# Performance work log

Hardware: AMD Instinct MI355X
Metric: run time of the kernel (lower is better)

## Reference

```python
import jax, jax.numpy as jnp
import numpy as np

N = 50000      # nodes
E = 800000     # edges
D_IN = 128
D_OUT = 128
R = 8          # relation types
EPS = 1e-12    # F.normalize eps


def setup_inputs() -> dict:
    key = jax.random.key(0)
    ks = jax.random.split(key, 10)
    s_in = 1.0 / np.sqrt(D_IN)
    s_out = 1.0 / np.sqrt(D_OUT)
    return {
        "x": jax.random.normal(ks[0], (N, D_IN), jnp.float32),
        "W1": jax.random.normal(ks[1], (R, D_IN, D_OUT), jnp.float32) * s_in,
        "loopW1": jax.random.normal(ks[2], (D_IN, D_OUT), jnp.float32) * s_in,
        "b1": jax.random.normal(ks[3], (D_OUT,), jnp.float32) * 0.01,
        "W2": jax.random.normal(ks[4], (R, D_OUT, D_OUT), jnp.float32) * s_out,
        "loopW2": jax.random.normal(ks[5], (D_OUT, D_OUT), jnp.float32) * s_out,
        "b2": jax.random.normal(ks[6], (D_OUT,), jnp.float32) * 0.01,
        "src": jax.random.randint(ks[7], (E,), 0, N),
        "dst": jax.random.randint(ks[8], (E,), 0, N),
        "etypes": jax.random.randint(ks[9], (E,), 0, R),
    }


def rel_layer(x, src, dst, etypes, W, loopW, b):
    # transform every node by every relation: [R, N, D_out]
    xw = jnp.einsum('ni,rio->rno', x, W)
    # gather per-edge messages: [E, D_out]
    msg = xw[etypes, src]
    # scatter-add to destination nodes
    agg = jax.ops.segment_sum(msg, dst, num_segments=x.shape[0])
    # self-loop + bias (DGL RelGraphConv defaults)
    return agg + x @ loopW + b


def reference(x, W1, loopW1, b1, W2, loopW2, b2, src, dst, etypes):
    h = jax.nn.relu(rel_layer(x, src, dst, etypes, W1, loopW1, b1))
    h = rel_layer(h, src, dst, etypes, W2, loopW2, b2)
    # F.normalize: row-wise L2, eps=1e-12
    nrm = jnp.maximum(jnp.linalg.norm(h, axis=1, keepdims=True), EPS)
    return h / nrm
```

## Files before the change

### kernel.cpp

```cpp
#include <hip/hip_runtime.h>
#include <hip/hip_bf16.h>

#define D 128
#define CH 4096
#define BM 64

typedef unsigned int u32;
typedef unsigned short u16;
typedef __attribute__((ext_vector_type(8))) short s16x8;
typedef __attribute__((ext_vector_type(4))) float f32x4;
typedef __attribute__((ext_vector_type(2))) float f32x2;

__device__ __forceinline__ float bf2f(u16 u) {
    union { u32 u; float f; } v; v.u = ((u32)u) << 16; return v.f;
}
__device__ __forceinline__ u16 f2bf(float f) {
    union { float f; u32 u; } v; v.f = f;
    return (u16)((v.u + 0x7fffu + ((v.u >> 16) & 1u)) >> 16);
}
__device__ __forceinline__ u32 pack_bf2(float a, float b) {
    __hip_bfloat162 t = __float22bfloat162_rn(make_float2(a, b));
    union { __hip_bfloat162 t; u32 u; } v; v.t = t; return v.u;
}
__device__ __forceinline__ void unpack2(u32 u, float& lo, float& hi) {
    union { u32 u; float f; } a, b;
    a.u = u << 16; b.u = u & 0xffff0000u;
    lo = a.f; hi = b.f;
}

__global__ void detect_dtype(const u16* __restrict__ x, int* __restrict__ flag,
                             int* __restrict__ gcnt, int nbuck) {
    __shared__ int cnt;
    if (threadIdx.x == 0) cnt = 0;
    __syncthreads();
    if ((int)threadIdx.x < nbuck) gcnt[threadIdx.x] = 0;
    u16 u = x[2 * threadIdx.x];
    int e = (u >> 7) & 0xFF;
    if (e >= 96 && e <= 150) atomicAdd(&cnt, 1);
    __syncthreads();
    if (threadIdx.x == 0) *flag = (cnt >= 128) ? 0 : 1;
}

__global__ __launch_bounds__(256)
void to_bf16_all(const void* __restrict__ s0, const void* __restrict__ s1,
                 const void* __restrict__ s2, const void* __restrict__ s3,
                 const void* __restrict__ s4, const void* __restrict__ s5,
                 const void* __restrict__ s6,
                 u16* __restrict__ d0, u16* __restrict__ d1, u16* __restrict__ d2,
                 u16* __restrict__ d3, u16* __restrict__ d4, u16* __restrict__ d5,
                 u16* __restrict__ d6,
                 long long n0, long long n1, long long n2, long long n3,
                 long long n4, long long n5, long long n6,
                 const int* __restrict__ flag)
{
    if (*flag == 0) return;
    long long i = (long long)blockIdx.x * 256 + threadIdx.x;
    const void* s; u16* d; long long off;
    if      (i < n0)                   { s = s0; d = d0; off = i; }
    else if (i < n0+n1)                { s = s1; d = d1; off = i-n0; }
    else if (i < n0+n1+n2)             { s = s2; d = d2; off = i-n0-n1; }
    else if (i < n0+n1+n2+n3)          { s = s3; d = d3; off = i-n0-n1-n2; }
    else if (i < n0+n1+n2+n3+n4)       { s = s4; d = d4; off = i-n0-n1-n2-n3; }
    else if (i < n0+n1+n2+n3+n4+n5)    { s = s5; d = d5; off = i-n0-n1-n2-n3-n4; }
    else if (i < n0+n1+n2+n3+n4+n5+n6) { s = s6; d = d6; off = i-n0-n1-n2-n3-n4-n5; }
    else return;
    d[off] = f2bf(((const float*)s)[off]);
}

__global__ __launch_bounds__(256)
void csr_count(const int* __restrict__ dst, int* __restrict__ gcnt, int E, int nbuck) {
    __shared__ int scnt[256];
    int tid = threadIdx.x;
    scnt[tid] = 0;
    __syncthreads();
    int base = blockIdx.x * CH;
#pragma unroll
    for (int it = 0; it < CH / 256; ++it) {
        int e = base + it * 256 + tid;
        if (e < E) atomicAdd(&scnt[dst[e] >> 8], 1);
    }
    __syncthreads();
    if (tid < nbuck && scnt[tid] > 0) atomicAdd(&gcnt[tid], scnt[tid]);
}

__global__ __launch_bounds__(256)
void csr_scan(const int* __restrict__ gcnt, int* __restrict__ bstart, int* __restrict__ bcur,
              int nbuck, int N_, int E_, int* __restrict__ offs) {
    __shared__ int wpart[4];
    int tid = threadIdx.x, lane = tid & 63, wid = tid >> 6;
    int v = (tid < nbuck) ? gcnt[tid] : 0;
    int s = v;
#pragma unroll
    for (int off = 1; off < 64; off <<= 1) {
        int t = __shfl_up(s, off, 64);
        if (lane >= off) s += t;
    }
    if (lane == 63) wpart[wid] = s;
    __syncthreads();
    int add = 0;
    for (int w = 0; w < wid; ++w) add += wpart[w];
    int excl = add + s - v;
    if (tid <= nbuck) bstart[tid] = excl;
    if (tid < nbuck)  bcur[tid]  = excl;
    if (tid == 0) offs[N_] = E_;
}

__global__ __launch_bounds__(256)
void csr_part(const int* __restrict__ src, const int* __restrict__ dst,
              const int* __restrict__ et, int* __restrict__ bcur,
              u32* __restrict__ ebuf, int E, int N, int nbuck) {
    __shared__ int scnt[256], sbase[256];
    int tid = threadIdx.x;
    scnt[tid] = 0;
    __syncthreads();
    int base = blockIdx.x * CH;
#pragma unroll
    for (int it = 0; it < CH / 256; ++it) {
        int e = base + it * 256 + tid;
        if (e < E) atomicAdd(&scnt[dst[e] >> 8], 1);
    }
    __syncthreads();
    if (tid < nbuck) {
        int c = scnt[tid];
        sbase[tid] = c ? atomicAdd(&bcur[tid], c) : 0;
    }
    __syncthreads();
    scnt[tid] = 0;
    __syncthreads();
#pragma unroll
    for (int it = 0; it < CH / 256; ++it) {
        int e = base + it * 256 + tid;
        if (e >= E) continue;
        int d = dst[e];
        int b = d >> 8;
        int p = sbase[b] + atomicAdd(&scnt[b], 1);
        ebuf[p] = ((u32)(d & 255) << 24) | ((u32)et[e] << 16) | (u32)src[e];
    }
}

__global__ __launch_bounds__(256)
void csr_emit(const u32* __restrict__ ebuf, const int* __restrict__ bstart,
              int* __restrict__ offs, int* __restrict__ rowidx, int N) {
    __shared__ int hist[256], excl[256], cur[256];
    __shared__ int wpart[4];
    int b = blockIdx.x, tid = threadIdx.x;
    int lo = bstart[b], hi = bstart[b + 1];
    hist[tid] = 0; cur[tid] = 0;
    __syncthreads();
    for (int i = lo + tid; i < hi; i += 256) atomicAdd(&hist[ebuf[i] >> 24], 1);
    __syncthreads();
    int lane = tid & 63, wid = tid >> 6;
    int v = hist[tid], s = v;
#pragma unroll
    for (int off = 1; off < 64; off <<= 1) {
        int t = __shfl_up(s, off, 64);
        if (lane >= off) s += t;
    }
    if (lane == 63) wpart[wid] = s;
    __syncthreads();
    int add = 0;
    for (int w = 0; w < wid; ++w) add += wpart[w];
    int e_ = add + s - v;
    excl[tid] = e_;
    int node = (b << 8) + tid;
    if (node < N) offs[node] = lo + e_;
    __syncthreads();
    for (int i = lo + tid; i < hi; i += 256) {
        u32 rec = ebuf[i];
        int dl = rec >> 24;
        int p = lo + excl[dl] + atomicAdd(&cur[dl], 1);
        rowidx[p] = (int)(rec & 0xFFFFFFu);
    }
}

#define ACC8(et_, u_) do { float l_, h_; unpack2((u_), l_, h_);        \
    switch (et_) {                                                     \
    case 0: aL[0] += l_; aH[0] += h_; break;                           \
    case 1: aL[1] += l_; aH[1] += h_; break;                           \
    case 2: aL[2] += l_; aH[2] += h_; break;                           \
    case 3: aL[3] += l_; aH[3] += h_; break;                           \
    case 4: aL[4] += l_; aH[4] += h_; break;                           \
    case 5: aL[5] += l_; aH[5] += h_; break;                           \
    case 6: aL[6] += l_; aH[6] += h_; break;                           \
    default: aL[7] += l_; aH[7] += h_; break; } } while (0)

__global__ __launch_bounds__(256)
void agg_pre(const u16* __restrict__ xc, const u16* __restrict__ xo,
             const int* __restrict__ offs, const int* __restrict__ rowidx,
             u16* __restrict__ s, int N_, int R_, const int* __restrict__ flag)
{
    const u16* x = (*flag != 0) ? xc : xo;
    int node = blockIdx.x * 4 + (threadIdx.x >> 6);
    int lane = threadIdx.x & 63;
    if (node >= N_) return;
    const u32* xr = (const u32*)x;

    float aL[8] = {0.f,0.f,0.f,0.f,0.f,0.f,0.f,0.f};
    float aH[8] = {0.f,0.f,0.f,0.f,0.f,0.f,0.f,0.f};

    int j  = __builtin_amdgcn_readfirstlane(offs[node]);
    int j1 = __builtin_amdgcn_readfirstlane(offs[node + 1]);

    for (; j + 4 <= j1; j += 4) {
        int v0 = __builtin_amdgcn_readfirstlane(rowidx[j + 0]);
        int v1 = __builtin_amdgcn_readfirstlane(rowidx[j + 1]);
        int v2 = __builtin_amdgcn_readfirstlane(rowidx[j + 2]);
        int v3 = __builtin_amdgcn_readfirstlane(rowidx[j + 3]);
        u32 u0 = xr[(size_t)(v0 & 0xffff) * 64 + lane];
        u32 u1 = xr[(size_t)(v1 & 0xffff) * 64 + lane];
        u32 u2 = xr[(size_t)(v2 & 0xffff) * 64 + lane];
        u32 u3 = xr[(size_t)(v3 & 0xffff) * 64 + lane];
        ACC8(v0 >> 16, u0);
        ACC8(v1 >> 16, u1);
        ACC8(v2 >> 16, u2);
        ACC8(v3 >> 16, u3);
    }
    for (; j < j1; ++j) {
        int v = __builtin_amdgcn_readfirstlane(rowidx[j]);
        u32 u = xr[(size_t)(v & 0xffff) * 64 + lane];
        ACC8(v >> 16, u);
    }

    size_t plane = (size_t)N_ * 64;
    u32* sp = (u32*)s + (size_t)node * 64 + lane;
#pragma unroll
    for (int r = 0; r < 8; ++r)
        if (r < R_) sp[(size_t)r * plane] = pack_bf2(aL[r], aH[r]);
}

__global__ __launch_bounds__(256)
void gemm_fused(const u16* __restrict__ s,
                const u16* __restrict__ selfc, const u16* __restrict__ selfo,
                const u16* __restrict__ Wc, const u16* __restrict__ Wo,
                const u16* __restrict__ lWc, const u16* __restrict__ lWo,
                const u16* __restrict__ bc, const u16* __restrict__ bo,
                const int* __restrict__ flag,
                int M, int R_, int mode, void* __restrict__ out)
{
    __shared__ u16 As[BM * 128];
    const bool f = (*flag != 0);
    const u16* self  = f ? selfc : selfo;
    const u16* Wall  = f ? Wc  : Wo;
    const u16* loopW = f ? lWc : lWo;
    const u16* bias  = f ? bc  : bo;

    const int row0 = blockIdx.x * BM;
    const int tid  = threadIdx.x;
    const int lane = tid & 63;
    const int wv   = tid >> 6;
    const int quad = lane >> 4;
    const int l16  = lane & 15;

    f32x4 acc[4][2];
#pragma unroll
    for (int mt = 0; mt < 4; ++mt) { acc[mt][0] = (f32x4)0.f; acc[mt][1] = (f32x4)0.f; }

    const size_t planeE = (size_t)M * D;
    const int r_base = (wv << 2) + (lane >> 4);
    const int ccol   = lane & 15;

    for (int c = 0; c <= R_; ++c) {
        const u16* Ak = (c < R_) ? (s + (size_t)c * planeE) : self;
        const u16* B  = (c < R_) ? (Wall + (size_t)c * D * D) : loopW;

        {
            auto* lds0 = (__attribute__((address_space(3))) char*)As;
            int cg = ccol ^ r_base;
            int rg0 = row0 + r_base;
#pragma unroll
            for (int it = 0; it < 4; ++it) {
                int rg = rg0 + it * 16; if (rg >= M) rg = M - 1;
                const u16* gp = Ak + (size_t)rg * D + cg * 8;
                __builtin_amdgcn_global_load_lds(
                    (const __attribute__((address_space(1))) void*)gp,
                    (__attribute__((address_space(3))) void*)(lds0 + it * 4096 + wv * 1024),
                    16, 0, 0);
            }
        }

        s16x8 bf[4][2];
#pragma unroll
        for (int ks = 0; ks < 4; ++ks)
#pragma unroll
            for (int jj = 0; jj < 8; ++jj) {
                u32 p = *(const u32*)(B + (ks * 32 + quad * 8 + jj) * D + wv * 32 + 2 * l16);
                bf[ks][0][jj] = (short)(p & 0xffffu);
                bf[ks][1][jj] = (short)(p >> 16);
            }

        __syncthreads();

#pragma unroll
        for (int ks = 0; ks < 4; ++ks) {
            const int chunk = (ks * 4 + quad) ^ l16;
#pragma unroll
            for (int mt = 0; mt < 4; ++mt) {
                s16x8 a = *(const s16x8*)(As + (mt * 16 + l16) * D + chunk * 8);
                acc[mt][0] = __builtin_amdgcn_mfma_f32_16x16x32_bf16(a, bf[ks][0], acc[mt][0], 0, 0, 0);
                acc[mt][1] = __builtin_amdgcn_mfma_f32_16x16x32_bf16(a, bf[ks][1], acc[mt][1], 0, 0, 0);
            }
        }
        __syncthreads();
    }

    const int cpair = wv * 16 + l16;
    const float b0 = bf2f(bias[2 * cpair]);
    const float b1 = bf2f(bias[2 * cpair + 1]);

    if (mode == 0) {
        u32* o = (u32*)out;
#pragma unroll
        for (int mt = 0; mt < 4; ++mt)
#pragma unroll
            for (int i = 0; i < 4; ++i) {
                int r = row0 + mt * 16 + quad * 4 + i;
                if (r >= M) continue;
                o[(size_t)r * 64 + cpair] = pack_bf2(fmaxf(acc[mt][0][i] + b0, 0.f),
                                                     fmaxf(acc[mt][1][i] + b1, 0.f));
            }
    } else {
        float pr[4][4];
#pragma unroll
        for (int mt = 0; mt < 4; ++mt)
#pragma unroll
            for (int i = 0; i < 4; ++i) {
                float a0 = acc[mt][0][i] + b0;
                float a1 = acc[mt][1][i] + b1;
                acc[mt][0][i] = a0; acc[mt][1][i] = a1;
                float p = a0 * a0 + a1 * a1;
                p += __shfl_xor(p, 1, 64);
                p += __shfl_xor(p, 2, 64);
                p += __shfl_xor(p, 4, 64);
                p += __shfl_xor(p, 8, 64);
                pr[mt][i] = p;
            }
        float* fs = (float*)As;
        if (l16 == 0) {
#pragma unroll
            for (int mt = 0; mt < 4; ++mt)
#pragma unroll
                for (int i = 0; i < 4; ++i)
                    fs[(mt * 16 + quad * 4 + i) * 4 + wv] = pr[mt][i];
        }
        __syncthreads();
        if (tid < 64) {
            float ssum = fs[tid * 4] + fs[tid * 4 + 1] + fs[tid * 4 + 2] + fs[tid * 4 + 3];
            fs[256 + tid] = 1.f / fmaxf(sqrtf(ssum), 1e-12f);
        }
        __syncthreads();
#pragma unroll
        for (int mt = 0; mt < 4; ++mt)
#pragma unroll
            for (int i = 0; i < 4; ++i) {
                int rl = mt * 16 + quad * 4 + i;
                int r = row0 + rl;
                if (r >= M) continue;
                float sc = fs[256 + rl];
                float a0 = acc[mt][0][i] * sc, a1 = acc[mt][1][i] * sc;
                if (f) {
                    f32x2 w; w[0] = a0; w[1] = a1;
                    ((f32x2*)out)[(size_t)r * 64 + cpair] = w;
                } else {
                    ((u32*)out)[(size_t)r * 64 + cpair] = pack_bf2(a0, a1);
                }
            }
    }
}

static inline size_t align256(size_t x) { return (x + 255) & ~(size_t)255; }

extern "C" void kernel_launch(void* const* d_in, const int* in_sizes, int n_in,
                              void* d_out, int out_size, void* d_ws, size_t ws_size,
                              hipStream_t stream)
{
    const void* x_in   = d_in[0];
    const void* W1_in  = d_in[1];
    const void* lW1_in = d_in[2];
    const void* b1_in  = d_in[3];
    const void* W2_in  = d_in[4];
    const void* lW2_in = d_in[5];
    const void* b2_in  = d_in[6];
    const int* src = (const int*)d_in[7];
    const int* dst = (const int*)d_in[8];
    const int* et  = (const int*)d_in[9];

    const int N = in_sizes[0] / D;
    const int E = in_sizes[7];
    const int R = in_sizes[1] / (D * D);
    const int nbuck = (N + 255) >> 8;

    const long long ND  = (long long)N * D;
    const long long RDD = (long long)R * D * D;
    const long long DDl = (long long)D * D;

    size_t off = 0;
    auto alloc = [&](size_t bytes) { size_t o = off; off = align256(off + bytes); return o; };
    size_t o_flag = alloc(256);
    size_t o_xc   = alloc((size_t)ND * 2);
    size_t o_W1   = alloc((size_t)RDD * 2);
    size_t o_lW1  = alloc((size_t)DDl * 2);
    size_t o_b1   = alloc((size_t)D * 2);
    size_t o_W2   = alloc((size_t)RDD * 2);
    size_t o_lW2  = alloc((size_t)DDl * 2);
    size_t o_b2   = alloc((size_t)D * 2);
    size_t o_h    = alloc((size_t)ND * 2);
    size_t o_offs = alloc((size_t)(N + 1) * 4);
    size_t o_gcnt = alloc(1024);
    size_t o_bst  = alloc(1040 * 4);
    size_t o_bcur = alloc(1024);
    size_t o_ebuf = alloc((size_t)E * 4);
    size_t o_ridx = alloc((size_t)E * 4);
    size_t o_s    = alloc((size_t)R * ND * 2);
    (void)ws_size;

    char* ws = (char*)d_ws;
    int* flag   = (int*)(ws + o_flag);
    u16* x_c    = (u16*)(ws + o_xc);
    u16* W1c    = (u16*)(ws + o_W1);
    u16* lW1c   = (u16*)(ws + o_lW1);
    u16* b1c    = (u16*)(ws + o_b1);
    u16* W2c    = (u16*)(ws + o_W2);
    u16* lW2c   = (u16*)(ws + o_lW2);
    u16* b2c    = (u16*)(ws + o_b2);
    u16* h      = (u16*)(ws + o_h);
    int* offs   = (int*)(ws + o_offs);
    int* gcnt   = (int*)(ws + o_gcnt);
    int* bstart = (int*)(ws + o_bst);
    int* bcur   = (int*)(ws + o_bcur);
    u32* ebuf   = (u32*)(ws + o_ebuf);
    int* rowidx = (int*)(ws + o_ridx);
    u16* sbuf   = (u16*)(ws + o_s);

    dim3 blk(256, 1, 1);
    int mb    = (N + BM - 1) / BM;
    int nblkE = (E + CH - 1) / CH;
    auto cdiv = [](long long n) { return (u32)((n + 255) / 256); };

    detect_dtype<<<dim3(1), blk, 0, stream>>>((const u16*)x_in, flag, gcnt, nbuck);
    long long tot = ND + RDD + DDl + D + RDD + DDl + D;
    to_bf16_all<<<dim3(cdiv(tot)), blk, 0, stream>>>(
        x_in, W1_in, lW1_in, b1_in, W2_in, lW2_in, b2_in,
        x_c, W1c, lW1c, b1c, W2c, lW2c, b2c,
        ND, RDD, DDl, (long long)D, RDD, DDl, (long long)D, flag);

    csr_count<<<dim3(nblkE), blk, 0, stream>>>(dst, gcnt, E, nbuck);
    csr_scan<<<dim3(1), blk, 0, stream>>>(gcnt, bstart, bcur, nbuck, N, E, offs);
    csr_part<<<dim3(nblkE), blk, 0, stream>>>(src, dst, et, bcur, ebuf, E, N, nbuck);
    csr_emit<<<dim3(nbuck), blk, 0, stream>>>(ebuf, bstart, offs, rowidx, N);

    agg_pre<<<dim3((N + 3) / 4), blk, 0, stream>>>(
        x_c, (const u16*)x_in, offs, rowidx, sbuf, N, R, flag);
    gemm_fused<<<dim3(mb), blk, 0, stream>>>(
        sbuf, x_c, (const u16*)x_in, W1c, (const u16*)W1_in, lW1c, (const u16*)lW1_in,
        b1c, (const u16*)b1_in, flag, N, R, 0, h);

    agg_pre<<<dim3((N + 3) / 4), blk, 0, stream>>>(
        h, h, offs, rowidx, sbuf, N, R, flag);
    gemm_fused<<<dim3(mb), blk, 0, stream>>>(
        sbuf, h, h, W2c, (const u16*)W2_in, lW2c, (const u16*)lW2_in,
        b2c, (const u16*)b2_in, flag, N, R, 1, d_out);
}
```

Before: 317.4 us.

## Fuse per-relation aggregation with the GEMM, staging sums in LDS

Merges the aggregation and GEMM kernels into one kernel per layer. Each 128-thread block gathers neighbor features for 32 rows into 8 swizzled LDS relation planes plus the self rows, then runs MFMA over all 9 planes. This removes the global round trip of the R×N×D bf16 intermediate and one launch per layer. In exchange it uses 72KB of LDS per block, which lowers occupancy, and the irregular gather now runs inside the GEMM block with fewer waves to hide latency.

```diff
diff --git a/kernel.cpp b/kernel.cpp
--- a/kernel.cpp
+++ b/kernel.cpp
@@ -3,7 +3,7 @@
 
 #define D 128
 #define CH 4096
-#define BM 64
+#define BM 32
 
 typedef unsigned int u32;
 typedef unsigned short u16;
@@ -184,65 +184,21 @@
     case 6: aL[6] += l_; aH[6] += h_; break;                           \
     default: aL[7] += l_; aH[7] += h_; break; } } while (0)
 
-__global__ __launch_bounds__(256)
-void agg_pre(const u16* __restrict__ xc, const u16* __restrict__ xo,
-             const int* __restrict__ offs, const int* __restrict__ rowidx,
-             u16* __restrict__ s, int N_, int R_, const int* __restrict__ flag)
+__global__ __launch_bounds__(128)
+void rel_layer_fused(const u16* __restrict__ xc, const u16* __restrict__ xo,
+                     const int* __restrict__ offs, const int* __restrict__ rowidx,
+                     const u16* __restrict__ Wc, const u16* __restrict__ Wo,
+                     const u16* __restrict__ lWc, const u16* __restrict__ lWo,
+                     const u16* __restrict__ bc, const u16* __restrict__ bo,
+                     const int* __restrict__ flag,
+                     int M, int R_, int mode, void* __restrict__ out)
 {
-    const u16* x = (*flag != 0) ? xc : xo;
-    int node = blockIdx.x * 4 + (threadIdx.x >> 6);
-    int lane = threadIdx.x & 63;
-    if (node >= N_) return;
-    const u32* xr = (const u32*)x;
-
-    float aL[8] = {0.f,0.f,0.f,0.f,0.f,0.f,0.f,0.f};
-    float aH[8] = {0.f,0.f,0.f,0.f,0.f,0.f,0.f,0.f};
-
-    int j  = __builtin_amdgcn_readfirstlane(offs[node]);
-    int j1 = __builtin_amdgcn_readfirstlane(offs[node + 1]);
-
-    for (; j + 4 <= j1; j += 4) {
-        int v0 = __builtin_amdgcn_readfirstlane(rowidx[j + 0]);
-        int v1 = __builtin_amdgcn_readfirstlane(rowidx[j + 1]);
-        int v2 = __builtin_amdgcn_readfirstlane(rowidx[j + 2]);
-        int v3 = __builtin_amdgcn_readfirstlane(rowidx[j + 3]);
-        u32 u0 = xr[(size_t)(v0 & 0xffff) * 64 + lane];
-        u32 u1 = xr[(size_t)(v1 & 0xffff) * 64 + lane];
-        u32 u2 = xr[(size_t)(v2 & 0xffff) * 64 + lane];
-        u32 u3 = xr[(size_t)(v3 & 0xffff) * 64 + lane];
-        ACC8(v0 >> 16, u0);
-        ACC8(v1 >> 16, u1);
-        ACC8(v2 >> 16, u2);
-        ACC8(v3 >> 16, u3);
-    }
-    for (; j < j1; ++j) {
-        int v = __builtin_amdgcn_readfirstlane(rowidx[j]);
-        u32 u = xr[(size_t)(v & 0xffff) * 64 + lane];
-        ACC8(v >> 16, u);
-    }
-
-    size_t plane = (size_t)N_ * 64;
-    u32* sp = (u32*)s + (size_t)node * 64 + lane;
-#pragma unroll
-    for (int r = 0; r < 8; ++r)
-        if (r < R_) sp[(size_t)r * plane] = pack_bf2(aL[r], aH[r]);
-}
-
-__global__ __launch_bounds__(256)
-void gemm_fused(const u16* __restrict__ s,
-                const u16* __restrict__ selfc, const u16* __restrict__ selfo,
-                const u16* __restrict__ Wc, const u16* __restrict__ Wo,
-                const u16* __restrict__ lWc, const u16* __restrict__ lWo,
-                const u16* __restrict__ bc, const u16* __restrict__ bo,
-                const int* __restrict__ flag,
-                int M, int R_, int mode, void* __restrict__ out)
-{
-    __shared__ u16 As[BM * 128];
+    __shared__ u16 As[9 * BM * D];
     const bool f = (*flag != 0);
-    const u16* self  = f ? selfc : selfo;
-    const u16* Wall  = f ? Wc  : Wo;
+    const u16* X     = f ? xc : xo;
+    const u16* Wall  = f ? Wc : Wo;
     const u16* loopW = f ? lWc : lWo;
-    const u16* bias  = f ? bc  : bo;
+    const u16* bias  = f ? bc : bo;
 
     const int row0 = blockIdx.x * BM;
     const int tid  = threadIdx.x;
@@ -251,117 +207,180 @@
     const int quad = lane >> 4;
     const int l16  = lane & 15;
 
-    f32x4 acc[4][2];
-#pragma unroll
-    for (int mt = 0; mt < 4; ++mt) { acc[mt][0] = (f32x4)0.f; acc[mt][1] = (f32x4)0.f; }
-
-    const size_t planeE = (size_t)M * D;
-    const int r_base = (wv << 2) + (lane >> 4);
-    const int ccol   = lane & 15;
+    {
+        auto* lds0 = (__attribute__((address_space(3))) char*)As;
+#pragma unroll
+        for (int it = 0; it < 4; ++it) {
+            int rl = it * 8 + wv * 4 + quad;
+            int cg = l16 ^ (rl & 15);
+            int rg = row0 + rl; if (rg >= M) rg = M - 1;
+            const u16* gp = X + (size_t)rg * D + cg * 8;
+            __builtin_amdgcn_global_load_lds(
+                (const __attribute__((address_space(1))) void*)gp,
+                (__attribute__((address_space(3))) void*)(lds0 + 65536 + (it * 8 + wv * 4) * 256),
+                16, 0, 0);
+        }
+    }
+
+    {
+        const u32* xr = (const u32*)X;
+        const int gbase = row0 + wv * 16;
+        int idx = gbase + lane; if (idx > M) idx = M;
+        int offv = offs[idx];
+        u32* plane = (u32*)As;
+
+        for (int rr = 0; rr < 16; ++rr) {
+            int j0 = __builtin_amdgcn_readlane(offv, rr);
+            int j1 = __builtin_amdgcn_readlane(offv, rr + 1);
+            float aL[8] = {0.f,0.f,0.f,0.f,0.f,0.f,0.f,0.f};
+            float aH[8] = {0.f,0.f,0.f,0.f,0.f,0.f,0.f,0.f};
+            int nE = j1 - j0;
+            if (nE > 0) {
+                int vcl = j0 + lane; if (vcl > j1 - 1) vcl = j1 - 1;
+                int vrow = rowidx[vcl];
+                int nb = nE < 64 ? nE : 64;
+                int kk = 0;
+                for (; kk + 8 <= nb; kk += 8) {
+                    int i0 = __builtin_amdgcn_readlane(vrow, kk + 0);
+                    int i1 = __builtin_amdgcn_readlane(vrow, kk + 1);
+                    int i2 = __builtin_amdgcn_readlane(vrow, kk + 2);
+                    int i3 = __builtin_amdgcn_readlane(vrow, kk + 3);
+                    int i4 = __builtin_amdgcn_readlane(vrow, kk + 4);
+                    int i5 = __builtin_amdgcn_readlane(vrow, kk + 5);
+                    int i6 = __builtin_amdgcn_readlane(vrow, kk + 6);
+                    int i7 = __builtin_amdgcn_readlane(vrow, kk + 7);
+                    u32 g0 = xr[(size_t)(i0 & 0xffff) * 64 + lane];
+                    u32 g1 = xr[(size_t)(i1 & 0xffff) * 64 + lane];
+                    u32 g2 = xr[(size_t)(i2 & 0xffff) * 64 + lane];
+                    u32 g3 = xr[(size_t)(i3 & 0xffff) * 64 + lane];
+                    u32 g4 = xr[(size_t)(i4 & 0xffff) * 64 + lane];
+                    u32 g5 = xr[(size_t)(i5 & 0xffff) * 64 + lane];
+                    u32 g6 = xr[(size_t)(i6 & 0xffff) * 64 + lane];
+                    u32 g7 = xr[(size_t)(i7 & 0xffff) * 64 + lane];
+                    ACC8(i0 >> 16, g0); ACC8(i1 >> 16, g1);
+                    ACC8(i2 >> 16, g2); ACC8(i3 >> 16, g3);
+                    ACC8(i4 >> 16, g4); ACC8(i5 >> 16, g5);
+                    ACC8(i6 >> 16, g6); ACC8(i7 >> 16, g7);
+                }
+                for (; kk < nb; ++kk) {
+                    int v = __builtin_amdgcn_readlane(vrow, kk);
+                    u32 g = xr[(size_t)(v & 0xffff) * 64 + lane];
+                    ACC8(v >> 16, g);
+                }
+                for (int j = j0 + 64; j < j1; ++j) {
+                    int v = __builtin_amdgcn_readfirstlane(rowidx[j]);
+                    u32 g = xr[(size_t)(v & 0xffff) * 64 + lane];
+                    ACC8(v >> 16, g);
+                }
+            }
+            int rl = wv * 16 + rr;
+            int widx = rl * 64 + (((lane >> 2) ^ rr) << 2) + (lane & 3);
+#pragma unroll
+            for (int r = 0; r < 8; ++r)
+                if (r < R_) plane[r * 2048 + widx] = pack_bf2(aL[r], aH[r]);
+        }
+    }
+
+    __syncthreads();
+
+    f32x4 acc[2][4];
+#pragma unroll
+    for (int mt = 0; mt < 2; ++mt)
+#pragma unroll
+        for (int q = 0; q < 4; ++q) acc[mt][q] = (f32x4)0.f;
 
     for (int c = 0; c <= R_; ++c) {
-        const u16* Ak = (c < R_) ? (s + (size_t)c * planeE) : self;
-        const u16* B  = (c < R_) ? (Wall + (size_t)c * D * D) : loopW;
-
-        {
-            auto* lds0 = (__attribute__((address_space(3))) char*)As;
-            int cg = ccol ^ r_base;
-            int rg0 = row0 + r_base;
-#pragma unroll
-            for (int it = 0; it < 4; ++it) {
-                int rg = rg0 + it * 16; if (rg >= M) rg = M - 1;
-                const u16* gp = Ak + (size_t)rg * D + cg * 8;
-                __builtin_amdgcn_global_load_lds(
-                    (const __attribute__((address_space(1))) void*)gp,
-                    (__attribute__((address_space(3))) void*)(lds0 + it * 4096 + wv * 1024),
-                    16, 0, 0);
+        const u16* B = (c < R_) ? (Wall + (size_t)c * D * D) : loopW;
+        const int pidx = (c < R_) ? c : 8;
+        s16x8 bfr[4][4];
+#pragma unroll
+        for (int ks = 0; ks < 4; ++ks)
+#pragma unroll
+            for (int g = 0; g < 2; ++g)
+#pragma unroll
+                for (int jj = 0; jj < 8; ++jj) {
+                    u32 p = *(const u32*)(B + (ks * 32 + quad * 8 + jj) * D + wv * 64 + g * 32 + 2 * l16);
+                    bfr[ks][2 * g][jj]     = (short)(p & 0xffffu);
+                    bfr[ks][2 * g + 1][jj] = (short)(p >> 16);
+                }
+#pragma unroll
+        for (int ks = 0; ks < 4; ++ks) {
+            const int chp = (ks * 4 + quad) ^ l16;
+#pragma unroll
+            for (int mt = 0; mt < 2; ++mt) {
+                s16x8 a = *(const s16x8*)(As + (pidx * BM + mt * 16 + l16) * D + chp * 8);
+#pragma unroll
+                for (int q = 0; q < 4; ++q)
+                    acc[mt][q] = __builtin_amdgcn_mfma_f32_16x16x32_bf16(a, bfr[ks][q], acc[mt][q], 0, 0, 0);
             }
         }
-
-        s16x8 bf[4][2];
-#pragma unroll
-        for (int ks = 0; ks < 4; ++ks)
-#pragma unroll
-            for (int jj = 0; jj < 8; ++jj) {
-                u32 p = *(const u32*)(B + (ks * 32 + quad * 8 + jj) * D + wv * 32 + 2 * l16);
-                bf[ks][0][jj] = (short)(p & 0xffffu);
-                bf[ks][1][jj] = (short)(p >> 16);
-            }
-
-        __syncthreads();
-
-#pragma unroll
-        for (int ks = 0; ks < 4; ++ks) {
-            const int chunk = (ks * 4 + quad) ^ l16;
-#pragma unroll
-            for (int mt = 0; mt < 4; ++mt) {
-                s16x8 a = *(const s16x8*)(As + (mt * 16 + l16) * D + chunk * 8);
-                acc[mt][0] = __builtin_amdgcn_mfma_f32_16x16x32_bf16(a, bf[ks][0], acc[mt][0], 0, 0, 0);
-                acc[mt][1] = __builtin_amdgcn_mfma_f32_16x16x32_bf16(a, bf[ks][1], acc[mt][1], 0, 0, 0);
-            }
-        }
-        __syncthreads();
-    }
-
-    const int cpair = wv * 16 + l16;
-    const float b0 = bf2f(bias[2 * cpair]);
-    const float b1 = bf2f(bias[2 * cpair + 1]);
+    }
+
+    const int cp0 = wv * 32 + l16;
+    const int cp1 = wv * 32 + 16 + l16;
+    const float b00 = bf2f(bias[2 * cp0]), b01 = bf2f(bias[2 * cp0 + 1]);
+    const float b10 = bf2f(bias[2 * cp1]), b11 = bf2f(bias[2 * cp1 + 1]);
 
     if (mode == 0) {
         u32* o = (u32*)out;
 #pragma unroll
-        for (int mt = 0; mt < 4; ++mt)
+        for (int mt = 0; mt < 2; ++mt)
 #pragma unroll
             for (int i = 0; i < 4; ++i) {
                 int r = row0 + mt * 16 + quad * 4 + i;
                 if (r >= M) continue;
-                o[(size_t)r * 64 + cpair] = pack_bf2(fmaxf(acc[mt][0][i] + b0, 0.f),
-                                                     fmaxf(acc[mt][1][i] + b1, 0.f));
+                o[(size_t)r * 64 + cp0] = pack_bf2(fmaxf(acc[mt][0][i] + b00, 0.f),
+                                                  fmaxf(acc[mt][1][i] + b01, 0.f));
+                o[(size_t)r * 64 + cp1] = pack_bf2(fmaxf(acc[mt][2][i] + b10, 0.f),
+                                                  fmaxf(acc[mt][3][i] + b11, 0.f));
             }
     } else {
-        float pr[4][4];
-#pragma unroll
-        for (int mt = 0; mt < 4; ++mt)
+        float* fs = (float*)As;
+        __syncthreads();
+        float pr[2][4];
+#pragma unroll
+        for (int mt = 0; mt < 2; ++mt)
 #pragma unroll
             for (int i = 0; i < 4; ++i) {
-                float a0 = acc[mt][0][i] + b0;
-                float a1 = acc[mt][1][i] + b1;
+                float a0 = acc[mt][0][i] + b00;
+                float a1 = acc[mt][1][i] + b01;
+                float a2 = acc[mt][2][i] + b10;
+                float a3 = acc[mt][3][i] + b11;
                 acc[mt][0][i] = a0; acc[mt][1][i] = a1;
-                float p = a0 * a0 + a1 * a1;
+                acc[mt][2][i] = a2; acc[mt][3][i] = a3;
+                float p = a0 * a0 + a1 * a1 + a2 * a2 + a3 * a3;
                 p += __shfl_xor(p, 1, 64);
                 p += __shfl_xor(p, 2, 64);
                 p += __shfl_xor(p, 4, 64);
                 p += __shfl_xor(p, 8, 64);
                 pr[mt][i] = p;
             }
-        float* fs = (float*)As;
         if (l16 == 0) {
 #pragma unroll
-            for (int mt = 0; mt < 4; ++mt)
+            for (int mt = 0; mt < 2; ++mt)
 #pragma unroll
                 for (int i = 0; i < 4; ++i)
-                    fs[(mt * 16 + quad * 4 + i) * 4 + wv] = pr[mt][i];
+                    fs[(mt * 16 + quad * 4 + i) * 2 + wv] = pr[mt][i];
         }
         __syncthreads();
-        if (tid < 64) {
-            float ssum = fs[tid * 4] + fs[tid * 4 + 1] + fs[tid * 4 + 2] + fs[tid * 4 + 3];
-            fs[256 + tid] = 1.f / fmaxf(sqrtf(ssum), 1e-12f);
-        }
-        __syncthreads();
-#pragma unroll
-        for (int mt = 0; mt < 4; ++mt)
+#pragma unroll
+        for (int mt = 0; mt < 2; ++mt)
 #pragma unroll
             for (int i = 0; i < 4; ++i) {
                 int rl = mt * 16 + quad * 4 + i;
                 int r = row0 + rl;
                 if (r >= M) continue;
-                float sc = fs[256 + rl];
+                float sc = 1.f / fmaxf(sqrtf(fs[rl * 2] + fs[rl * 2 + 1]), 1e-12f);
                 float a0 = acc[mt][0][i] * sc, a1 = acc[mt][1][i] * sc;
+                float a2 = acc[mt][2][i] * sc, a3 = acc[mt][3][i] * sc;
                 if (f) {
-                    f32x2 w; w[0] = a0; w[1] = a1;
-                    ((f32x2*)out)[(size_t)r * 64 + cpair] = w;
+                    f32x2 w0; w0[0] = a0; w0[1] = a1;
+                    f32x2 w1; w1[0] = a2; w1[1] = a3;
+                    ((f32x2*)out)[(size_t)r * 64 + cp0] = w0;
+                    ((f32x2*)out)[(size_t)r * 64 + cp1] = w1;
                 } else {
-                    ((u32*)out)[(size_t)r * 64 + cpair] = pack_bf2(a0, a1);
+                    ((u32*)out)[(size_t)r * 64 + cp0] = pack_bf2(a0, a1);
+                    ((u32*)out)[(size_t)r * 64 + cp1] = pack_bf2(a2, a3);
                 }
             }
     }
@@ -410,7 +429,6 @@
     size_t o_bcur = alloc(1024);
     size_t o_ebuf = alloc((size_t)E * 4);
     size_t o_ridx = alloc((size_t)E * 4);
-    size_t o_s    = alloc((size_t)R * ND * 2);
     (void)ws_size;
 
     char* ws = (char*)d_ws;
@@ -429,7 +447,6 @@
     int* bcur   = (int*)(ws + o_bcur);
     u32* ebuf   = (u32*)(ws + o_ebuf);
     int* rowidx = (int*)(ws + o_ridx);
-    u16* sbuf   = (u16*)(ws + o_s);
 
     dim3 blk(256, 1, 1);
     int mb    = (N + BM - 1) / BM;
@@ -448,15 +465,13 @@
     csr_part<<<dim3(nblkE), blk, 0, stream>>>(src, dst, et, bcur, ebuf, E, N, nbuck);
     csr_emit<<<dim3(nbuck), blk, 0, stream>>>(ebuf, bstart, offs, rowidx, N);
 
-    agg_pre<<<dim3((N + 3) / 4), blk, 0, stream>>>(
-        x_c, (const u16*)x_in, offs, rowidx, sbuf, N, R, flag);
-    gemm_fused<<<dim3(mb), blk, 0, stream>>>(
-        sbuf, x_c, (const u16*)x_in, W1c, (const u16*)W1_in, lW1c, (const u16*)lW1_in,
+    rel_layer_fused<<<dim3(mb), dim3(128), 0, stream>>>(
+        x_c, (const u16*)x_in, offs, rowidx,
+        W1c, (const u16*)W1_in, lW1c, (const u16*)lW1_in,
         b1c, (const u16*)b1_in, flag, N, R, 0, h);
 
-    agg_pre<<<dim3((N + 3) / 4), blk, 0, stream>>>(
-        h, h, offs, rowidx, sbuf, N, R, flag);
-    gemm_fused<<<dim3(mb), blk, 0, stream>>>(
-        sbuf, h, h, W2c, (const u16*)W2_in, lW2c, (const u16*)lW2_in,
+    rel_layer_fused<<<dim3(mb), dim3(128), 0, stream>>>(
+        h, h, offs, rowidx,
+        W2c, (const u16*)W2_in, lW2c, (const u16*)lW2_in,
         b2c, (const u16*)b2_in, flag, N, R, 1, d_out);
 }
```

Result: slower. 628.2 us (+98.0%).

## Fuse per-relation aggregation into GEMM kernel with etype-sorted CSR and pre-swizzled weights

Applied to the files above, without the earlier changes.

Drops the separate agg_pre kernel and its global per-relation staging buffer. Each rel_layer_fused block now aggregates neighbour features for its 16 rows directly into LDS planes, one per relation, then runs MFMA over the 9 weight matrices. The CSR is additionally sorted by edge type within each destination, so each wave can accumulate runs and flush once per type change. A build_wt kernel pre-swizzles the weights into the MFMA fragment layout so B loads become vectorized. This removes the large bf16 intermediate written and read through HBM, at the cost of smaller GEMM tiles, more LDS per block and serial gather loops per wave.

```diff
diff --git a/kernel.cpp b/kernel.cpp
--- a/kernel.cpp
+++ b/kernel.cpp
@@ -3,7 +3,7 @@
 
 #define D 128
 #define CH 4096
-#define BM 64
+#define BM 16
 
 typedef unsigned int u32;
 typedef unsigned short u16;
@@ -141,16 +141,23 @@
 __global__ __launch_bounds__(256)
 void csr_emit(const u32* __restrict__ ebuf, const int* __restrict__ bstart,
               int* __restrict__ offs, int* __restrict__ rowidx, int N) {
-    __shared__ int hist[256], excl[256], cur[256];
+    __shared__ int hist[2048], excl[2048], cur[2048];
     __shared__ int wpart[4];
     int b = blockIdx.x, tid = threadIdx.x;
     int lo = bstart[b], hi = bstart[b + 1];
-    hist[tid] = 0; cur[tid] = 0;
-    __syncthreads();
-    for (int i = lo + tid; i < hi; i += 256) atomicAdd(&hist[ebuf[i] >> 24], 1);
-    __syncthreads();
+    for (int i = tid; i < 2048; i += 256) { hist[i] = 0; cur[i] = 0; }
+    __syncthreads();
+    for (int i = lo + tid; i < hi; i += 256) {
+        u32 rec = ebuf[i];
+        int key = (int)((rec >> 24) << 3) | (int)((rec >> 16) & 7u);
+        atomicAdd(&hist[key], 1);
+    }
+    __syncthreads();
+    int loc[8]; int tsum = 0;
+#pragma unroll
+    for (int k = 0; k < 8; ++k) { loc[k] = tsum; tsum += hist[tid * 8 + k]; }
     int lane = tid & 63, wid = tid >> 6;
-    int v = hist[tid], s = v;
+    int s = tsum;
 #pragma unroll
     for (int off = 1; off < 64; off <<= 1) {
         int t = __shfl_up(s, off, 64);
@@ -160,89 +167,64 @@
     __syncthreads();
     int add = 0;
     for (int w = 0; w < wid; ++w) add += wpart[w];
-    int e_ = add + s - v;
-    excl[tid] = e_;
+    int tex = add + s - tsum;
+#pragma unroll
+    for (int k = 0; k < 8; ++k) excl[tid * 8 + k] = tex + loc[k];
     int node = (b << 8) + tid;
-    if (node < N) offs[node] = lo + e_;
+    if (node < N) offs[node] = lo + tex;
     __syncthreads();
     for (int i = lo + tid; i < hi; i += 256) {
         u32 rec = ebuf[i];
-        int dl = rec >> 24;
-        int p = lo + excl[dl] + atomicAdd(&cur[dl], 1);
+        int key = (int)((rec >> 24) << 3) | (int)((rec >> 16) & 7u);
+        int p = lo + excl[key] + atomicAdd(&cur[key], 1);
         rowidx[p] = (int)(rec & 0xFFFFFFu);
     }
 }
 
-#define ACC8(et_, u_) do { float l_, h_; unpack2((u_), l_, h_);        \
-    switch (et_) {                                                     \
-    case 0: aL[0] += l_; aH[0] += h_; break;                           \
-    case 1: aL[1] += l_; aH[1] += h_; break;                           \
-    case 2: aL[2] += l_; aH[2] += h_; break;                           \
-    case 3: aL[3] += l_; aH[3] += h_; break;                           \
-    case 4: aL[4] += l_; aH[4] += h_; break;                           \
-    case 5: aL[5] += l_; aH[5] += h_; break;                           \
-    case 6: aL[6] += l_; aH[6] += h_; break;                           \
-    default: aL[7] += l_; aH[7] += h_; break; } } while (0)
-
 __global__ __launch_bounds__(256)
-void agg_pre(const u16* __restrict__ xc, const u16* __restrict__ xo,
-             const int* __restrict__ offs, const int* __restrict__ rowidx,
-             u16* __restrict__ s, int N_, int R_, const int* __restrict__ flag)
+void build_wt(const u16* __restrict__ W1c, const u16* __restrict__ W1o,
+              const u16* __restrict__ lW1c, const u16* __restrict__ lW1o,
+              const u16* __restrict__ W2c, const u16* __restrict__ W2o,
+              const u16* __restrict__ lW2c, const u16* __restrict__ lW2o,
+              const int* __restrict__ flag, int R_, u16* __restrict__ wt)
 {
-    const u16* x = (*flag != 0) ? xc : xo;
-    int node = blockIdx.x * 4 + (threadIdx.x >> 6);
-    int lane = threadIdx.x & 63;
-    if (node >= N_) return;
-    const u32* xr = (const u32*)x;
-
-    float aL[8] = {0.f,0.f,0.f,0.f,0.f,0.f,0.f,0.f};
-    float aH[8] = {0.f,0.f,0.f,0.f,0.f,0.f,0.f,0.f};
-
-    int j  = __builtin_amdgcn_readfirstlane(offs[node]);
-    int j1 = __builtin_amdgcn_readfirstlane(offs[node + 1]);
-
-    for (; j + 4 <= j1; j += 4) {
-        int v0 = __builtin_amdgcn_readfirstlane(rowidx[j + 0]);
-        int v1 = __builtin_amdgcn_readfirstlane(rowidx[j + 1]);
-        int v2 = __builtin_amdgcn_readfirstlane(rowidx[j + 2]);
-        int v3 = __builtin_amdgcn_readfirstlane(rowidx[j + 3]);
-        u32 u0 = xr[(size_t)(v0 & 0xffff) * 64 + lane];
-        u32 u1 = xr[(size_t)(v1 & 0xffff) * 64 + lane];
-        u32 u2 = xr[(size_t)(v2 & 0xffff) * 64 + lane];
-        u32 u3 = xr[(size_t)(v3 & 0xffff) * 64 + lane];
-        ACC8(v0 >> 16, u0);
-        ACC8(v1 >> 16, u1);
-        ACC8(v2 >> 16, u2);
-        ACC8(v3 >> 16, u3);
-    }
-    for (; j < j1; ++j) {
-        int v = __builtin_amdgcn_readfirstlane(rowidx[j]);
-        u32 u = xr[(size_t)(v & 0xffff) * 64 + lane];
-        ACC8(v >> 16, u);
-    }
-
-    size_t plane = (size_t)N_ * 64;
-    u32* sp = (u32*)s + (size_t)node * 64 + lane;
-#pragma unroll
-    for (int r = 0; r < 8; ++r)
-        if (r < R_) sp[(size_t)r * plane] = pack_bf2(aL[r], aH[r]);
-}
-
-__global__ __launch_bounds__(256)
-void gemm_fused(const u16* __restrict__ s,
-                const u16* __restrict__ selfc, const u16* __restrict__ selfo,
-                const u16* __restrict__ Wc, const u16* __restrict__ Wo,
-                const u16* __restrict__ lWc, const u16* __restrict__ lWo,
-                const u16* __restrict__ bc, const u16* __restrict__ bo,
-                const int* __restrict__ flag,
-                int M, int R_, int mode, void* __restrict__ out)
+    __shared__ u32 st[8192];
+    bool f = (*flag != 0);
+    int m = blockIdx.x;
+    int layer = m / 9, c = m % 9;
+    const u16* src;
+    if (layer == 0) src = (c < R_) ? ((f ? W1c : W1o) + (size_t)c * D * D) : (f ? lW1c : lW1o);
+    else            src = (c < R_) ? ((f ? W2c : W2o) + (size_t)c * D * D) : (f ? lW2c : lW2o);
+    int tid = threadIdx.x;
+    const u32* s32 = (const u32*)src;
+    for (int i = tid; i < 8192; i += 256) st[i] = s32[i];
+    __syncthreads();
+    const u16* st16 = (const u16*)st;
+    u16* dstp = wt + (size_t)m * 16384;
+    for (int i = tid; i < 16384; i += 256) {
+        int wvv = i >> 12;
+        int ks  = (i >> 10) & 3;
+        int h   = (i >> 9) & 1;
+        int ln  = (i >> 3) & 63;
+        int j   = i & 7;
+        int k   = ks * 32 + (ln >> 4) * 8 + j;
+        int col = wvv * 32 + 2 * (ln & 15) + h;
+        dstp[i] = st16[k * 128 + col];
+    }
+}
+
+__global__ __launch_bounds__(256, 4)
+void rel_layer_fused(const u16* __restrict__ xc, const u16* __restrict__ xo,
+                     const int* __restrict__ offs, const int* __restrict__ rowidx,
+                     const u16* __restrict__ wt,
+                     const u16* __restrict__ bc, const u16* __restrict__ bo,
+                     const int* __restrict__ flag,
+                     int M, int R_, int mode, void* __restrict__ out)
 {
-    __shared__ u16 As[BM * 128];
+    __shared__ u16 As[9 * BM * D];
     const bool f = (*flag != 0);
-    const u16* self  = f ? selfc : selfo;
-    const u16* Wall  = f ? Wc  : Wo;
-    const u16* loopW = f ? lWc : lWo;
-    const u16* bias  = f ? bc  : bo;
+    const u16* X    = f ? xc : xo;
+    const u16* bias = f ? bc : bo;
 
     const int row0 = blockIdx.x * BM;
     const int tid  = threadIdx.x;
@@ -251,119 +233,183 @@
     const int quad = lane >> 4;
     const int l16  = lane & 15;
 
-    f32x4 acc[4][2];
-#pragma unroll
-    for (int mt = 0; mt < 4; ++mt) { acc[mt][0] = (f32x4)0.f; acc[mt][1] = (f32x4)0.f; }
-
-    const size_t planeE = (size_t)M * D;
-    const int r_base = (wv << 2) + (lane >> 4);
-    const int ccol   = lane & 15;
-
-    for (int c = 0; c <= R_; ++c) {
-        const u16* Ak = (c < R_) ? (s + (size_t)c * planeE) : self;
-        const u16* B  = (c < R_) ? (Wall + (size_t)c * D * D) : loopW;
-
-        {
-            auto* lds0 = (__attribute__((address_space(3))) char*)As;
-            int cg = ccol ^ r_base;
-            int rg0 = row0 + r_base;
-#pragma unroll
-            for (int it = 0; it < 4; ++it) {
-                int rg = rg0 + it * 16; if (rg >= M) rg = M - 1;
-                const u16* gp = Ak + (size_t)rg * D + cg * 8;
-                __builtin_amdgcn_global_load_lds(
-                    (const __attribute__((address_space(1))) void*)gp,
-                    (__attribute__((address_space(3))) void*)(lds0 + it * 4096 + wv * 1024),
-                    16, 0, 0);
+    {
+        auto* lds0 = (__attribute__((address_space(3))) char*)As;
+        int rl = wv * 4 + quad;
+        int rg = row0 + rl; if (rg >= M) rg = M - 1;
+        int cg = l16 ^ rl;
+        const u16* gp = X + (size_t)rg * D + cg * 8;
+        __builtin_amdgcn_global_load_lds(
+            (const __attribute__((address_space(1))) void*)gp,
+            (__attribute__((address_space(3))) void*)(lds0 + 8 * BM * 256 + wv * 1024),
+            16, 0, 0);
+    }
+
+    {
+        u32* pz = (u32*)As;
+        int rbase = wv * 4;
+#pragma unroll
+        for (int pl = 0; pl < 8; ++pl)
+#pragma unroll
+            for (int rr = 0; rr < 4; ++rr)
+                pz[(pl * BM + rbase + rr) * 64 + lane] = 0;
+    }
+
+    {
+        const u32* X32 = (const u32*)X;
+        u32* plane = (u32*)As;
+        int v0 = row0 + wv * 4;
+        int idx = v0 + lane; if (idx > M) idx = M;
+        int offv = offs[idx];
+        int jbase = __builtin_amdgcn_readlane(offv, 0);
+        int jend  = __builtin_amdgcn_readlane(offv, 4);
+        int nE = jend - jbase;
+        if (nE > 0 && nE <= 128) {
+            int vrow = rowidx[(jbase + lane < jend) ? jbase + lane : jend - 1];
+            int vrow2 = 0;
+            if (nE > 64) vrow2 = rowidx[(jbase + 64 + lane < jend) ? jbase + 64 + lane : jend - 1];
+            int rowptr = 0;
+            int rnext = __builtin_amdgcn_readlane(offv, 1);
+            int rl = wv * 4;
+            int vsw = (((lane >> 2) ^ rl) << 2) | (lane & 3);
+            int rcur = -1;
+            float a0 = 0.f, a1 = 0.f;
+            int j = jbase;
+            while (j < jend) {
+                int nb = jend - j; if (nb > 8) nb = 8;
+                int rec[8]; u32 g[8];
+#pragma unroll
+                for (int k = 0; k < 8; ++k) {
+                    if (k < nb) {
+                        int kk = j - jbase + k;
+                        rec[k] = (kk < 64) ? __builtin_amdgcn_readlane(vrow, kk)
+                                           : __builtin_amdgcn_readlane(vrow2, kk - 64);
+                    }
+                }
+#pragma unroll
+                for (int k = 0; k < 8; ++k)
+                    if (k < nb) g[k] = X32[(size_t)(rec[k] & 0xffff) * 64 + lane];
+#pragma unroll
+                for (int k = 0; k < 8; ++k) {
+                    if (k < nb) {
+                        int jj = j + k;
+                        while (jj >= rnext) {
+                            if (rcur >= 0) {
+                                plane[(rcur * BM + rl) * 64 + vsw] = pack_bf2(a0, a1);
+                                rcur = -1; a0 = 0.f; a1 = 0.f;
+                            }
+                            rowptr++;
+                            rl = wv * 4 + rowptr;
+                            vsw = (((lane >> 2) ^ rl) << 2) | (lane & 3);
+                            rnext = __builtin_amdgcn_readlane(offv, rowptr + 1);
+                        }
+                        int et = rec[k] >> 16;
+                        if (et != rcur) {
+                            if (rcur >= 0) plane[(rcur * BM + rl) * 64 + vsw] = pack_bf2(a0, a1);
+                            rcur = et; a0 = 0.f; a1 = 0.f;
+                        }
+                        float lo_, hi_;
+                        unpack2(g[k], lo_, hi_);
+                        a0 += lo_; a1 += hi_;
+                    }
+                }
+                j += nb;
+            }
+            if (rcur >= 0) plane[(rcur * BM + rl) * 64 + vsw] = pack_bf2(a0, a1);
+        } else if (nE > 128) {
+            for (int rr = 0; rr < 4; ++rr) {
+                int j0 = __builtin_amdgcn_readlane(offv, rr);
+                int j1 = __builtin_amdgcn_readlane(offv, rr + 1);
+                int rl = wv * 4 + rr;
+                int vsw = (((lane >> 2) ^ rl) << 2) | (lane & 3);
+                int rcur = -1; float a0 = 0.f, a1 = 0.f;
+                for (int j = j0; j < j1; ++j) {
+                    u32 rec = (u32)rowidx[j];
+                    int et = (int)(rec >> 16);
+                    if (et != rcur) {
+                        if (rcur >= 0) plane[(rcur * BM + rl) * 64 + vsw] = pack_bf2(a0, a1);
+                        rcur = et; a0 = 0.f; a1 = 0.f;
+                    }
+                    float lo_, hi_;
+                    unpack2(X32[(size_t)(rec & 0xffff) * 64 + lane], lo_, hi_);
+                    a0 += lo_; a1 += hi_;
+                }
+                if (rcur >= 0) plane[(rcur * BM + rl) * 64 + vsw] = pack_bf2(a0, a1);
             }
         }
-
-        s16x8 bf[4][2];
+    }
+
+    __syncthreads();
+
+    f32x4 acc[2];
+    acc[0] = (f32x4)0.f; acc[1] = (f32x4)0.f;
+    for (int c = 0; c <= R_; ++c) {
+        int cidx = (c < R_) ? c : 8;
+        const u16* Bt = wt + (size_t)cidx * 16384 + (size_t)wv * 4096 + lane * 8;
+        s16x8 bfr[4][2];
 #pragma unroll
         for (int ks = 0; ks < 4; ++ks)
 #pragma unroll
-            for (int jj = 0; jj < 8; ++jj) {
-                u32 p = *(const u32*)(B + (ks * 32 + quad * 8 + jj) * D + wv * 32 + 2 * l16);
-                bf[ks][0][jj] = (short)(p & 0xffffu);
-                bf[ks][1][jj] = (short)(p >> 16);
-            }
-
+            for (int h = 0; h < 2; ++h)
+                bfr[ks][h] = *(const s16x8*)(Bt + (ks * 2 + h) * 512);
+#pragma unroll
+        for (int ks = 0; ks < 4; ++ks) {
+            int chp = (ks * 4 + quad) ^ l16;
+            s16x8 a = *(const s16x8*)(As + (cidx * BM + l16) * D + chp * 8);
+            acc[0] = __builtin_amdgcn_mfma_f32_16x16x32_bf16(a, bfr[ks][0], acc[0], 0, 0, 0);
+            acc[1] = __builtin_amdgcn_mfma_f32_16x16x32_bf16(a, bfr[ks][1], acc[1], 0, 0, 0);
+        }
+    }
+
+    const int cp = wv * 16 + l16;
+    const float b0 = bf2f(bias[2 * cp]);
+    const float b1 = bf2f(bias[2 * cp + 1]);
+
+    if (mode == 0) {
+        u32* o = (u32*)out;
+#pragma unroll
+        for (int i = 0; i < 4; ++i) {
+            int r = row0 + quad * 4 + i;
+            if (r >= M) continue;
+            o[(size_t)r * 64 + cp] = pack_bf2(fmaxf(acc[0][i] + b0, 0.f),
+                                              fmaxf(acc[1][i] + b1, 0.f));
+        }
+    } else {
         __syncthreads();
-
-#pragma unroll
-        for (int ks = 0; ks < 4; ++ks) {
-            const int chunk = (ks * 4 + quad) ^ l16;
-#pragma unroll
-            for (int mt = 0; mt < 4; ++mt) {
-                s16x8 a = *(const s16x8*)(As + (mt * 16 + l16) * D + chunk * 8);
-                acc[mt][0] = __builtin_amdgcn_mfma_f32_16x16x32_bf16(a, bf[ks][0], acc[mt][0], 0, 0, 0);
-                acc[mt][1] = __builtin_amdgcn_mfma_f32_16x16x32_bf16(a, bf[ks][1], acc[mt][1], 0, 0, 0);
+        float* fs = (float*)As;
+        float pr[4];
+#pragma unroll
+        for (int i = 0; i < 4; ++i) {
+            float a0 = acc[0][i] + b0;
+            float a1 = acc[1][i] + b1;
+            acc[0][i] = a0; acc[1][i] = a1;
+            float p = a0 * a0 + a1 * a1;
+            p += __shfl_xor(p, 1, 64);
+            p += __shfl_xor(p, 2, 64);
+            p += __shfl_xor(p, 4, 64);
+            p += __shfl_xor(p, 8, 64);
+            pr[i] = p;
+        }
+        if (l16 == 0) {
+#pragma unroll
+            for (int i = 0; i < 4; ++i) fs[(quad * 4 + i) * 4 + wv] = pr[i];
+        }
+        __syncthreads();
+#pragma unroll
+        for (int i = 0; i < 4; ++i) {
+            int rl = quad * 4 + i;
+            int r = row0 + rl;
+            if (r >= M) continue;
+            float ssum = fs[rl * 4] + fs[rl * 4 + 1] + fs[rl * 4 + 2] + fs[rl * 4 + 3];
+            float sc = 1.f / fmaxf(sqrtf(ssum), 1e-12f);
+            float a0 = acc[0][i] * sc, a1 = acc[1][i] * sc;
+            if (f) {
+                f32x2 w; w[0] = a0; w[1] = a1;
+                ((f32x2*)out)[(size_t)r * 64 + cp] = w;
+            } else {
+                ((u32*)out)[(size_t)r * 64 + cp] = pack_bf2(a0, a1);
             }
         }
-        __syncthreads();
-    }
-
-    const int cpair = wv * 16 + l16;
-    const float b0 = bf2f(bias[2 * cpair]);
-    const float b1 = bf2f(bias[2 * cpair + 1]);
-
-    if (mode == 0) {
-        u32* o = (u32*)out;
-#pragma unroll
-        for (int mt = 0; mt < 4; ++mt)
-#pragma unroll
-            for (int i = 0; i < 4; ++i) {
-                int r = row0 + mt * 16 + quad * 4 + i;
-                if (r >= M) continue;
-                o[(size_t)r * 64 + cpair] = pack_bf2(fmaxf(acc[mt][0][i] + b0, 0.f),
-                                                     fmaxf(acc[mt][1][i] + b1, 0.f));
-            }
-    } else {
-        float pr[4][4];
-#pragma unroll
-        for (int mt = 0; mt < 4; ++mt)
-#pragma unroll
-            for (int i = 0; i < 4; ++i) {
-                float a0 = acc[mt][0][i] + b0;
-                float a1 = acc[mt][1][i] + b1;
-                acc[mt][0][i] = a0; acc[mt][1][i] = a1;
-                float p = a0 * a0 + a1 * a1;
-                p += __shfl_xor(p, 1, 64);
-                p += __shfl_xor(p, 2, 64);
-                p += __shfl_xor(p, 4, 64);
-                p += __shfl_xor(p, 8, 64);
-                pr[mt][i] = p;
-            }
-        float* fs = (float*)As;
-        if (l16 == 0) {
-#pragma unroll
-            for (int mt = 0; mt < 4; ++mt)
-#pragma unroll
-                for (int i = 0; i < 4; ++i)
-                    fs[(mt * 16 + quad * 4 + i) * 4 + wv] = pr[mt][i];
-        }
-        __syncthreads();
-        if (tid < 64) {
-            float ssum = fs[tid * 4] + fs[tid * 4 + 1] + fs[tid * 4 + 2] + fs[tid * 4 + 3];
-            fs[256 + tid] = 1.f / fmaxf(sqrtf(ssum), 1e-12f);
-        }
-        __syncthreads();
-#pragma unroll
-        for (int mt = 0; mt < 4; ++mt)
-#pragma unroll
-            for (int i = 0; i < 4; ++i) {
-                int rl = mt * 16 + quad * 4 + i;
-                int r = row0 + rl;
-                if (r >= M) continue;
-                float sc = fs[256 + rl];
-                float a0 = acc[mt][0][i] * sc, a1 = acc[mt][1][i] * sc;
-                if (f) {
-                    f32x2 w; w[0] = a0; w[1] = a1;
-                    ((f32x2*)out)[(size_t)r * 64 + cpair] = w;
-                } else {
-                    ((u32*)out)[(size_t)r * 64 + cpair] = pack_bf2(a0, a1);
-                }
-            }
     }
 }
 
@@ -410,7 +456,7 @@
     size_t o_bcur = alloc(1024);
     size_t o_ebuf = alloc((size_t)E * 4);
     size_t o_ridx = alloc((size_t)E * 4);
-    size_t o_s    = alloc((size_t)R * ND * 2);
+    size_t o_wt   = alloc((size_t)2 * 9 * D * D * 2);
     (void)ws_size;
 
     char* ws = (char*)d_ws;
@@ -429,7 +475,7 @@
     int* bcur   = (int*)(ws + o_bcur);
     u32* ebuf   = (u32*)(ws + o_ebuf);
     int* rowidx = (int*)(ws + o_ridx);
-    u16* sbuf   = (u16*)(ws + o_s);
+    u16* wt     = (u16*)(ws + o_wt);
 
     dim3 blk(256, 1, 1);
     int mb    = (N + BM - 1) / BM;
@@ -443,20 +489,20 @@
         x_c, W1c, lW1c, b1c, W2c, lW2c, b2c,
         ND, RDD, DDl, (long long)D, RDD, DDl, (long long)D, flag);
 
+    build_wt<<<dim3(18), blk, 0, stream>>>(
+        W1c, (const u16*)W1_in, lW1c, (const u16*)lW1_in,
+        W2c, (const u16*)W2_in, lW2c, (const u16*)lW2_in, flag, R, wt);
+
     csr_count<<<dim3(nblkE), blk, 0, stream>>>(dst, gcnt, E, nbuck);
     csr_scan<<<dim3(1), blk, 0, stream>>>(gcnt, bstart, bcur, nbuck, N, E, offs);
     csr_part<<<dim3(nblkE), blk, 0, stream>>>(src, dst, et, bcur, ebuf, E, N, nbuck);
     csr_emit<<<dim3(nbuck), blk, 0, stream>>>(ebuf, bstart, offs, rowidx, N);
 
-    agg_pre<<<dim3((N + 3) / 4), blk, 0, stream>>>(
-        x_c, (const u16*)x_in, offs, rowidx, sbuf, N, R, flag);
-    gemm_fused<<<dim3(mb), blk, 0, stream>>>(
-        sbuf, x_c, (const u16*)x_in, W1c, (const u16*)W1_in, lW1c, (const u16*)lW1_in,
+    rel_layer_fused<<<dim3(mb), blk, 0, stream>>>(
+        x_c, (const u16*)x_in, offs, rowidx, wt,
         b1c, (const u16*)b1_in, flag, N, R, 0, h);
 
-    agg_pre<<<dim3((N + 3) / 4), blk, 0, stream>>>(
-        h, h, offs, rowidx, sbuf, N, R, flag);
-    gemm_fused<<<dim3(mb), blk, 0, stream>>>(
-        sbuf, h, h, W2c, (const u16*)W2_in, lW2c, (const u16*)lW2_in,
+    rel_layer_fused<<<dim3(mb), blk, 0, stream>>>(
+        h, h, offs, rowidx, wt + (size_t)9 * D * D,
         b2c, (const u16*)b2_in, flag, N, R, 1, d_out);
 }
```

After: 438.6 us. +38.2%, slower.
